# Kernel optimization log

Measured on AMD Instinct MI355X. Metric: run time of the kernel, lower is better.

The kernel has to match this reference:

```python
import jax, jax.numpy as jnp
import numpy as np

TEMP = 0.7
ALPHA_ADV = 1.0
BETA_BAND = 0.5
BAND_L = 0.05
BAND_H = 0.2
W_HEUR = 0.5
W_LEAR = 0.5


def setup_inputs() -> dict:
    key = jax.random.key(0)
    ks = jax.random.split(key, 6)
    B, Sn, C, H, W = 2, 5, 64, 192, 192
    hid = 64
    return {
        "S": jax.random.normal(ks[0], (B, C, H, W), jnp.float32),
        "T": jax.random.normal(ks[1], (B, Sn, C, H, W), jnp.float32),
        "adapt_w": jax.random.normal(ks[2], (Sn, C, C), jnp.float32) / np.sqrt(C).astype(np.float32),
        "adapt_b": jnp.zeros((Sn, C), jnp.float32),
        "r_w1": jax.random.normal(ks[3], (hid, Sn * C * 3), jnp.float32) * 0.05,
        "r_b1": jnp.zeros((hid,), jnp.float32),
        "r_w2": jax.random.normal(ks[4], (Sn, hid), jnp.float32) * 0.05,
        "r_b2": jnp.zeros((Sn,), jnp.float32),
        "ema_mu": jnp.zeros((1, Sn, C, 1, 1), jnp.float32),
        "ema_sigma": jnp.ones((1, Sn, C, 1, 1), jnp.float32),
        "ema_proxy": jnp.zeros((1, Sn, 1, 1, 1), jnp.float32),
    }


def reference(S, T, adapt_w, adapt_b, r_w1, r_b1, r_w2, r_b2, ema_mu, ema_sigma, ema_proxy):
    B, Sn, C, H, W = T.shape
    bias = adapt_b[None, :, :, None, None]
    # per-sweep 1x1 conv == per-sweep channel matmul
    T_adapt = jnp.einsum('sdc,bschw->bsdhw', adapt_w, T) + bias          # [B,S,C,H,W]
    S_rep = jnp.einsum('sdc,bchw->bsdhw', adapt_w, S) + bias             # [B,S,C,H,W]
    Tz = (T_adapt - ema_mu) / ema_sigma
    Sz = (S_rep - ema_mu) / ema_sigma
    delta = Tz - Sz
    proxy = jnp.mean(delta * delta, axis=2, keepdims=True)               # [B,S,1,H,W]
    cur = jnp.mean(proxy, axis=(0, 3, 4), keepdims=True)                 # [1,S,1,1,1]
    # heuristic score (gamma_ucb = 0 -> no UCB term)
    impr = jax.lax.stop_gradient(ema_proxy - cur)
    adv = impr - jnp.mean(impr, axis=1, keepdims=True)
    below = jnp.maximum(BAND_L - cur, 0.0)
    above = jnp.maximum(cur - BAND_H, 0.0)
    band = -(below * below + above * above)
    score = ALPHA_ADV * adv + BETA_BAND * band                           # [1,S,1,1,1]
    score_heur = jnp.broadcast_to(score, proxy.shape)[:, :, 0]           # [B,S,H,W]
    # learned router: concat along channel of each sweep then 1x1 MLP
    x = jnp.concatenate([Sz, Tz, delta], axis=2).reshape(B, Sn * 3 * C, H, W)
    h = jax.nn.relu(jnp.einsum('oi,bihw->bohw', r_w1, x) + r_b1[None, :, None, None])
    score_learn = jnp.einsum('oi,bihw->bohw', r_w2, h) + r_b2[None, :, None, None]
    logits = W_HEUR * score_heur + W_LEAR * score_learn                  # [B,S,H,W]
    weights = jax.nn.softmax(logits / TEMP, axis=1)                      # soft gating over sweeps
    return weights
```

## Files before the change

### kernel.cpp

```cpp
#include <hip/hip_runtime.h>
#include <math.h>

#define HWSZ 36864
#define NBLK4 1152

typedef short bf16x8 __attribute__((ext_vector_type(8)));
typedef float f32x16 __attribute__((ext_vector_type(16)));
typedef unsigned int u32x4 __attribute__((ext_vector_type(4)));

__device__ __forceinline__ unsigned short f2bf(float x) {
    unsigned u = __float_as_uint(x);
    return (unsigned short)((u + 0x7fffu + ((u >> 16) & 1u)) >> 16);
}

__device__ __forceinline__ void block_sync_lds() {
    __builtin_amdgcn_sched_barrier(0);
    asm volatile("s_waitcnt lgkmcnt(0)" ::: "memory");
    __builtin_amdgcn_s_barrier();
    __builtin_amdgcn_sched_barrier(0);
}

__global__ void pre_all(const float* __restrict__ rw1, const float* __restrict__ rb1,
                        const float* __restrict__ aw, const float* __restrict__ ab,
                        const float* __restrict__ mu, const float* __restrict__ sg,
                        unsigned short* __restrict__ AfragW,
                        unsigned short* __restrict__ AfragMS2, float* __restrict__ c1) {
    int i = blockIdx.x * 256 + threadIdx.x;
    if (i < 40960) {
        int s = i / 8192, rem = i % 8192;
        int r = rem / 2048, rem2 = rem % 2048;
        int t = rem2 / 512, q = rem2 % 512;
        int l = q >> 3, e = q & 7;
        int R = 32 * r + (l & 31);
        int k = 16 * t + 8 * (l >> 5) + e;
        float v;
        if (R < 64) {
            v = aw[s * 4096 + R * 64 + k] / sg[s * 64 + R];
        } else {
            int o = R - 64;
            const float* wp = rw1 + o * 960 + s * 192;
            const float* A  = aw + s * 4096 + k;
            const float* G  = sg + s * 64;
            float sum = 0.f;
            #pragma unroll 8
            for (int d = 0; d < 64; ++d)
                sum = fmaf(wp[64 + d] + wp[128 + d], A[d * 64] / G[d], sum);
            v = sum;
        }
        AfragW[i] = f2bf(v);
    } else if (i < 45056) {
        int j = i - 40960;
        int r = j / 2048, rem2 = j % 2048;
        int t = rem2 / 512, q = rem2 % 512;
        int l = q >> 3, e = q & 7;
        int o = 32 * r + (l & 31);
        int k = 16 * t + 8 * (l >> 5) + e;
        float sum = 0.f;
        for (int s = 0; s < 5; ++s) {
            const float* wp = rw1 + o * 960 + s * 192;
            const float* A  = aw + s * 4096 + k;
            const float* G  = sg + s * 64;
            #pragma unroll 8
            for (int d = 0; d < 64; ++d)
                sum = fmaf(wp[d] - wp[128 + d], A[d * 64] / G[d], sum);
        }
        AfragMS2[j] = f2bf(sum);
    } else if (i < 45120) {
        int o = i - 45056;
        float sum = rb1[o];
        for (int s = 0; s < 5; ++s) {
            const float* wp = rw1 + o * 960 + s * 192;
            #pragma unroll 8
            for (int d = 0; d < 64; ++d) {
                int sd = s * 64 + d;
                sum = fmaf(wp[d] + wp[64 + d], (ab[sd] - mu[sd]) / sg[sd], sum);
            }
        }
        c1[o] = sum;
    }
}

__global__ __launch_bounds__(256, 4) void fused_main(
        const float* __restrict__ S, const float* __restrict__ T,
        const unsigned short* __restrict__ AfragW, const unsigned short* __restrict__ AfragMS2,
        const float* __restrict__ c1, const float* __restrict__ rw2, const float* __restrict__ rb2,
        float* __restrict__ slearn, float* __restrict__ partial) {
    __shared__ __align__(16) unsigned short sTile[4096];
    __shared__ __align__(16) unsigned short tbuf[2][4096];
    __shared__ float hpart[2][5][64];
    __shared__ float wred[5][2];
    __shared__ float w2s[320];
    __shared__ float c1s[64];
    __shared__ float rb2s[8];

    const int tid = threadIdx.x, lane = tid & 63, w = tid >> 6;
    const int hi = lane >> 5, pxm = lane & 31;
    const int blk = blockIdx.x;
    const int b = blk / 576;
    const int pix0 = (blk % 576) * 64;

    const int o8 = tid >> 5, q = tid & 31;
    const int skt = o8 >> 1, shh = o8 & 1;
    const float* Sp = S + ((size_t)(b * 64 + 8 * o8)) * HWSZ + pix0 + 2 * q;
    const float* Tp = T + ((size_t)(b * 5 * 64 + 8 * o8)) * HWSZ + pix0 + 2 * q;

    float2 RS[8], RA[8], RB[8];
    #pragma unroll
    for (int j = 0; j < 8; ++j) RS[j] = *(const float2*)(Sp + (size_t)j * HWSZ);
    #pragma unroll
    for (int j = 0; j < 8; ++j) RA[j] = *(const float2*)(Tp + (size_t)j * HWSZ);
    #pragma unroll
    for (int j = 0; j < 8; ++j) RB[j] = *(const float2*)(Tp + (size_t)(64 + j) * HWSZ);

    for (int i = tid; i < 320; i += 256) w2s[i] = rw2[i];
    if (tid < 64) c1s[tid] = c1[tid];
    if (tid < 5)  rb2s[tid] = rb2[tid];

    auto packWrite = [&](unsigned short* dst, const float2* Rv) {
        #pragma unroll
        for (int h2 = 0; h2 < 2; ++h2) {
            int px = 2 * q + h2;
            int ct = px >> 5, slot = (px & 31) ^ ct;
            u32x4 v;
            #pragma unroll
            for (int jj = 0; jj < 4; ++jj) {
                float a = h2 ? Rv[2 * jj].y : Rv[2 * jj].x;
                float c = h2 ? Rv[2 * jj + 1].y : Rv[2 * jj + 1].x;
                v[jj] = (unsigned)f2bf(a) | ((unsigned)f2bf(c) << 16);
            }
            *(u32x4*)&dst[(((ct * 4 + skt) * 64) + shh * 32 + slot) * 8] = v;
        }
    };
    auto loadT = [&](float2* Rv, int s) {
        const float* p = Tp + (size_t)(s * 64) * HWSZ;
        #pragma unroll
        for (int j = 0; j < 8; ++j) Rv[j] = *(const float2*)(p + (size_t)j * HWSZ);
    };

    const bf16x8* afw = (const bf16x8*)AfragW + lane;
    bf16x8 fr0[4], fr1[4];
    #pragma unroll
    for (int kt = 0; kt < 4; ++kt) fr0[kt] = afw[((0 * 4 + w) * 4 + kt) * 64];

    packWrite(sTile, RS);
    block_sync_lds();

    auto ldsB = [&](const unsigned short* buf, int ct, int kt) -> bf16x8 {
        return *(const bf16x8*)&buf[(((ct * 4 + kt) * 64) + hi * 32 + (pxm ^ ct)) * 8];
    };

    f32x16 acc0, acc1;
    #pragma unroll
    for (int i = 0; i < 16; ++i) { acc0[i] = 0.f; acc1[i] = 0.f; }

    if (w >= 2) {
        const bf16x8* am = (const bf16x8*)AfragMS2 + lane;
        bf16x8 ms2f[4];
        #pragma unroll
        for (int kt = 0; kt < 4; ++kt) ms2f[kt] = am[((w - 2) * 4 + kt) * 64];
        #pragma unroll
        for (int kt = 0; kt < 4; ++kt) {
            acc0 = __builtin_amdgcn_mfma_f32_32x32x16_bf16(ms2f[kt], ldsB(sTile, 0, kt), acc0, 0, 0, 0);
            acc1 = __builtin_amdgcn_mfma_f32_32x32x16_bf16(ms2f[kt], ldsB(sTile, 1, kt), acc1, 0, 0, 0);
        }
    }

    packWrite(tbuf[0], RA);
    loadT(RA, 2);
    block_sync_lds();

    #pragma unroll
    for (int s = 0; s < 5; ++s) {
        const unsigned short* cur = tbuf[s & 1];
        unsigned short* nxt = tbuf[(s + 1) & 1];
        bf16x8* fcur = (s & 1) ? fr1 : fr0;
        bf16x8* fnxt = (s & 1) ? fr0 : fr1;
        if (s < 4) {
            #pragma unroll
            for (int kt = 0; kt < 4; ++kt) fnxt[kt] = afw[(((s + 1) * 4 + w) * 4 + kt) * 64];
        }
        if (w < 2) {
            #pragma unroll
            for (int i = 0; i < 16; ++i) { acc0[i] = 0.f; acc1[i] = 0.f; }
            #pragma unroll
            for (int kt = 0; kt < 4; ++kt) {
                acc0 = __builtin_amdgcn_mfma_f32_32x32x16_bf16(fcur[kt], ldsB(sTile, 0, kt), acc0, 0, 0, 0);
                acc1 = __builtin_amdgcn_mfma_f32_32x32x16_bf16(fcur[kt], ldsB(sTile, 1, kt), acc1, 0, 0, 0);
            }
            #pragma unroll
            for (int i = 0; i < 16; ++i) { acc0[i] = -acc0[i]; acc1[i] = -acc1[i]; }
            #pragma unroll
            for (int kt = 0; kt < 4; ++kt) {
                acc0 = __builtin_amdgcn_mfma_f32_32x32x16_bf16(fcur[kt], ldsB(cur, 0, kt), acc0, 0, 0, 0);
                acc1 = __builtin_amdgcn_mfma_f32_32x32x16_bf16(fcur[kt], ldsB(cur, 1, kt), acc1, 0, 0, 0);
            }
            float sq = 0.f;
            #pragma unroll
            for (int i = 0; i < 16; ++i) { sq = fmaf(acc0[i], acc0[i], sq); sq = fmaf(acc1[i], acc1[i], sq); }
            #pragma unroll
            for (int m = 1; m < 64; m <<= 1) sq += __shfl_xor(sq, m, 64);
            if (lane == 0) wred[s][w] = sq;
        } else {
            #pragma unroll
            for (int kt = 0; kt < 4; ++kt) {
                acc0 = __builtin_amdgcn_mfma_f32_32x32x16_bf16(fcur[kt], ldsB(cur, 0, kt), acc0, 0, 0, 0);
                acc1 = __builtin_amdgcn_mfma_f32_32x32x16_bf16(fcur[kt], ldsB(cur, 1, kt), acc1, 0, 0, 0);
            }
        }
        if (s < 4) {
            packWrite(nxt, (s & 1) ? RA : RB);
            if (s < 2) loadT((s & 1) ? RA : RB, s + 3);
        }
        block_sync_lds();
    }

    if (w >= 2) {
        #pragma unroll
        for (int i = 0; i < 16; ++i) {
            int row = (i & 3) + 8 * (i >> 2) + 4 * hi + 32 * (w - 2);
            acc0[i] = fmaxf(acc0[i] + c1s[row], 0.f);
            acc1[i] = fmaxf(acc1[i] + c1s[row], 0.f);
        }
        #pragma unroll
        for (int sp = 0; sp < 5; ++sp) {
            float d0 = 0.f, d1 = 0.f;
            #pragma unroll
            for (int i = 0; i < 16; ++i) {
                int row = (i & 3) + 8 * (i >> 2) + 4 * hi + 32 * (w - 2);
                d0 = fmaf(w2s[sp * 64 + row], acc0[i], d0);
                d1 = fmaf(w2s[sp * 64 + row], acc1[i], d1);
            }
            d0 += __shfl_xor(d0, 32, 64);
            d1 += __shfl_xor(d1, 32, 64);
            if (hi == 0) { hpart[w - 2][sp][pxm] = d0; hpart[w - 2][sp][32 + pxm] = d1; }
        }
    }
    block_sync_lds();
    if (tid < 5) partial[blk * 5 + tid] = wred[tid][0] + wred[tid][1];
    for (int i = tid; i < 320; i += 256) {
        int sp = i >> 6, px = i & 63;
        slearn[((size_t)(b * 5 + sp)) * HWSZ + pix0 + px] =
            hpart[0][sp][px] + hpart[1][sp][px] + rb2s[sp];
    }
}

__global__ void score_kernel(const float* __restrict__ partial,
                             const float* __restrict__ ema_proxy,
                             float* __restrict__ scoreBuf) {
    __shared__ float red[256];
    __shared__ float cur[5];
    int tid = threadIdx.x;
    for (int s = 0; s < 5; ++s) {
        float sum = 0.f;
        for (int i = tid; i < NBLK4; i += 256) sum += partial[i * 5 + s];
        red[tid] = sum;
        __syncthreads();
        for (int off = 128; off > 0; off >>= 1) {
            if (tid < off) red[tid] += red[tid + off];
            __syncthreads();
        }
        if (tid == 0) cur[s] = red[0] * (1.0f / (64.0f * 2.0f * HWSZ));
        __syncthreads();
    }
    if (tid == 0) {
        float impr[5]; float m = 0.f;
        for (int s = 0; s < 5; ++s) { impr[s] = ema_proxy[s] - cur[s]; m += impr[s]; }
        m *= 0.2f;
        for (int s = 0; s < 5; ++s) {
            float adv = impr[s] - m;
            float c = cur[s];
            float below = fmaxf(0.05f - c, 0.f);
            float above = fmaxf(c - 0.2f, 0.f);
            float band = -(below * below + above * above);
            scoreBuf[s] = 1.0f * adv + 0.5f * band;
        }
    }
}

__global__ void softmax_kernel(const float* __restrict__ slearn,
                               const float* __restrict__ scoreBuf,
                               float* __restrict__ out) {
    int i = blockIdx.x * 256 + threadIdx.x;
    if (i >= 2 * HWSZ) return;
    int b = i / HWSZ, p = i % HWSZ;
    float l[5];
    float mx = -1e30f;
    #pragma unroll
    for (int s = 0; s < 5; ++s) {
        float v = (0.5f * scoreBuf[s] + 0.5f * slearn[((size_t)(b * 5 + s)) * HWSZ + p]) / 0.7f;
        l[s] = v;
        mx = fmaxf(mx, v);
    }
    float sum = 0.f;
    #pragma unroll
    for (int s = 0; s < 5; ++s) { l[s] = expf(l[s] - mx); sum += l[s]; }
    float inv = 1.0f / sum;
    #pragma unroll
    for (int s = 0; s < 5; ++s) out[((size_t)(b * 5 + s)) * HWSZ + p] = l[s] * inv;
}

extern "C" void kernel_launch(void* const* d_in, const int* in_sizes, int n_in,
                              void* d_out, int out_size, void* d_ws, size_t ws_size,
                              hipStream_t stream) {
    const float* S   = (const float*)d_in[0];
    const float* T   = (const float*)d_in[1];
    const float* aw  = (const float*)d_in[2];
    const float* ab  = (const float*)d_in[3];
    const float* rw1 = (const float*)d_in[4];
    const float* rb1 = (const float*)d_in[5];
    const float* rw2 = (const float*)d_in[6];
    const float* rb2 = (const float*)d_in[7];
    const float* mu  = (const float*)d_in[8];
    const float* sg  = (const float*)d_in[9];
    const float* ep  = (const float*)d_in[10];

    float* ws = (float*)d_ws;
    float* c1f      = ws;
    float* scoreBuf = ws + 64;
    float* partial  = ws + 72;
    unsigned short* AfragW   = (unsigned short*)(ws + 5832);
    unsigned short* AfragMS2 = (unsigned short*)(ws + 26312);
    float* slearn   = ws + 28360;
    float* out = (float*)d_out;

    pre_all<<<177, 256, 0, stream>>>(rw1, rb1, aw, ab, mu, sg, AfragW, AfragMS2, c1f);
    fused_main<<<NBLK4, 256, 0, stream>>>(S, T, AfragW, AfragMS2, c1f, rw2, rb2, slearn, partial);
    score_kernel<<<1, 256, 0, stream>>>(partial, ep, scoreBuf);
    softmax_kernel<<<288, 256, 0, stream>>>(slearn, scoreBuf, out);
}
```

Before: 58.04 us.

## Double pixel tile per block to 128 with float4 loads and 4 MFMA accumulators

Each block of the fused kernel now covers 128 pixels instead of 64. That halves the grid to 576 blocks and gives each block four 32-pixel MFMA column tiles, so every loaded weight fragment feeds four MFMAs instead of two. Global loads widen from float2 to float4, and the T prefetch drops from two register buffers to a single rotating buffer. LDS roughly doubles, hpart is aliased onto tbuf, and launch bounds fall to 3 blocks per SM, which reduces occupancy and the number of blocks available to spread across the device.

```diff
diff --git a/kernel.cpp b/kernel.cpp
--- a/kernel.cpp
+++ b/kernel.cpp
@@ -2,7 +2,8 @@
 #include <math.h>
 
 #define HWSZ 36864
-#define NBLK4 1152
+#define NPX  128
+#define NBLK5 576
 
 typedef short bf16x8 __attribute__((ext_vector_type(8)));
 typedef float f32x16 __attribute__((ext_vector_type(16)));
@@ -80,14 +81,13 @@
     }
 }
 
-__global__ __launch_bounds__(256, 4) void fused_main(
+__global__ __launch_bounds__(256, 3) void fused_main(
         const float* __restrict__ S, const float* __restrict__ T,
         const unsigned short* __restrict__ AfragW, const unsigned short* __restrict__ AfragMS2,
         const float* __restrict__ c1, const float* __restrict__ rw2, const float* __restrict__ rb2,
         float* __restrict__ slearn, float* __restrict__ partial) {
-    __shared__ __align__(16) unsigned short sTile[4096];
-    __shared__ __align__(16) unsigned short tbuf[2][4096];
-    __shared__ float hpart[2][5][64];
+    __shared__ __align__(16) unsigned short sTile[8192];
+    __shared__ __align__(16) unsigned short tbuf[2][8192];
     __shared__ float wred[5][2];
     __shared__ float w2s[320];
     __shared__ float c1s[64];
@@ -96,45 +96,43 @@
     const int tid = threadIdx.x, lane = tid & 63, w = tid >> 6;
     const int hi = lane >> 5, pxm = lane & 31;
     const int blk = blockIdx.x;
-    const int b = blk / 576;
-    const int pix0 = (blk % 576) * 64;
+    const int b = blk / 288;
+    const int pix0 = (blk % 288) * NPX;
 
     const int o8 = tid >> 5, q = tid & 31;
     const int skt = o8 >> 1, shh = o8 & 1;
-    const float* Sp = S + ((size_t)(b * 64 + 8 * o8)) * HWSZ + pix0 + 2 * q;
-    const float* Tp = T + ((size_t)(b * 5 * 64 + 8 * o8)) * HWSZ + pix0 + 2 * q;
-
-    float2 RS[8], RA[8], RB[8];
-    #pragma unroll
-    for (int j = 0; j < 8; ++j) RS[j] = *(const float2*)(Sp + (size_t)j * HWSZ);
-    #pragma unroll
-    for (int j = 0; j < 8; ++j) RA[j] = *(const float2*)(Tp + (size_t)j * HWSZ);
-    #pragma unroll
-    for (int j = 0; j < 8; ++j) RB[j] = *(const float2*)(Tp + (size_t)(64 + j) * HWSZ);
+    const float* Sp = S + ((size_t)(b * 64 + 8 * o8)) * HWSZ + pix0 + 4 * q;
+    const float* Tp = T + ((size_t)(b * 5 * 64 + 8 * o8)) * HWSZ + pix0 + 4 * q;
+
+    float4 RS[8], RA[8];
+    #pragma unroll
+    for (int j = 0; j < 8; ++j) RS[j] = *(const float4*)(Sp + (size_t)j * HWSZ);
+    #pragma unroll
+    for (int j = 0; j < 8; ++j) RA[j] = *(const float4*)(Tp + (size_t)j * HWSZ);
 
     for (int i = tid; i < 320; i += 256) w2s[i] = rw2[i];
     if (tid < 64) c1s[tid] = c1[tid];
     if (tid < 5)  rb2s[tid] = rb2[tid];
 
-    auto packWrite = [&](unsigned short* dst, const float2* Rv) {
-        #pragma unroll
-        for (int h2 = 0; h2 < 2; ++h2) {
-            int px = 2 * q + h2;
+    auto packWrite = [&](unsigned short* dst, const float4* Rv) {
+        #pragma unroll
+        for (int pi = 0; pi < 4; ++pi) {
+            int px = 4 * q + pi;
             int ct = px >> 5, slot = (px & 31) ^ ct;
             u32x4 v;
             #pragma unroll
             for (int jj = 0; jj < 4; ++jj) {
-                float a = h2 ? Rv[2 * jj].y : Rv[2 * jj].x;
-                float c = h2 ? Rv[2 * jj + 1].y : Rv[2 * jj + 1].x;
+                float a = ((const float*)&Rv[2 * jj])[pi];
+                float c = ((const float*)&Rv[2 * jj + 1])[pi];
                 v[jj] = (unsigned)f2bf(a) | ((unsigned)f2bf(c) << 16);
             }
             *(u32x4*)&dst[(((ct * 4 + skt) * 64) + shh * 32 + slot) * 8] = v;
         }
     };
-    auto loadT = [&](float2* Rv, int s) {
+    auto loadT = [&](float4* Rv, int s) {
         const float* p = Tp + (size_t)(s * 64) * HWSZ;
         #pragma unroll
-        for (int j = 0; j < 8; ++j) Rv[j] = *(const float2*)(p + (size_t)j * HWSZ);
+        for (int j = 0; j < 8; ++j) Rv[j] = *(const float4*)(p + (size_t)j * HWSZ);
     };
 
     const bf16x8* afw = (const bf16x8*)AfragW + lane;
@@ -149,9 +147,11 @@
         return *(const bf16x8*)&buf[(((ct * 4 + kt) * 64) + hi * 32 + (pxm ^ ct)) * 8];
     };
 
-    f32x16 acc0, acc1;
-    #pragma unroll
-    for (int i = 0; i < 16; ++i) { acc0[i] = 0.f; acc1[i] = 0.f; }
+    f32x16 acc[4];
+    #pragma unroll
+    for (int n = 0; n < 4; ++n)
+        #pragma unroll
+        for (int i = 0; i < 16; ++i) acc[n][i] = 0.f;
 
     if (w >= 2) {
         const bf16x8* am = (const bf16x8*)AfragMS2 + lane;
@@ -159,14 +159,14 @@
         #pragma unroll
         for (int kt = 0; kt < 4; ++kt) ms2f[kt] = am[((w - 2) * 4 + kt) * 64];
         #pragma unroll
-        for (int kt = 0; kt < 4; ++kt) {
-            acc0 = __builtin_amdgcn_mfma_f32_32x32x16_bf16(ms2f[kt], ldsB(sTile, 0, kt), acc0, 0, 0, 0);
-            acc1 = __builtin_amdgcn_mfma_f32_32x32x16_bf16(ms2f[kt], ldsB(sTile, 1, kt), acc1, 0, 0, 0);
-        }
+        for (int kt = 0; kt < 4; ++kt)
+            #pragma unroll
+            for (int n = 0; n < 4; ++n)
+                acc[n] = __builtin_amdgcn_mfma_f32_32x32x16_bf16(ms2f[kt], ldsB(sTile, n, kt), acc[n], 0, 0, 0);
     }
 
     packWrite(tbuf[0], RA);
-    loadT(RA, 2);
+    loadT(RA, 1);
     block_sync_lds();
 
     #pragma unroll
@@ -181,66 +181,74 @@
         }
         if (w < 2) {
             #pragma unroll
-            for (int i = 0; i < 16; ++i) { acc0[i] = 0.f; acc1[i] = 0.f; }
-            #pragma unroll
-            for (int kt = 0; kt < 4; ++kt) {
-                acc0 = __builtin_amdgcn_mfma_f32_32x32x16_bf16(fcur[kt], ldsB(sTile, 0, kt), acc0, 0, 0, 0);
-                acc1 = __builtin_amdgcn_mfma_f32_32x32x16_bf16(fcur[kt], ldsB(sTile, 1, kt), acc1, 0, 0, 0);
-            }
-            #pragma unroll
-            for (int i = 0; i < 16; ++i) { acc0[i] = -acc0[i]; acc1[i] = -acc1[i]; }
-            #pragma unroll
-            for (int kt = 0; kt < 4; ++kt) {
-                acc0 = __builtin_amdgcn_mfma_f32_32x32x16_bf16(fcur[kt], ldsB(cur, 0, kt), acc0, 0, 0, 0);
-                acc1 = __builtin_amdgcn_mfma_f32_32x32x16_bf16(fcur[kt], ldsB(cur, 1, kt), acc1, 0, 0, 0);
-            }
+            for (int n = 0; n < 4; ++n)
+                #pragma unroll
+                for (int i = 0; i < 16; ++i) acc[n][i] = 0.f;
+            #pragma unroll
+            for (int kt = 0; kt < 4; ++kt)
+                #pragma unroll
+                for (int n = 0; n < 4; ++n)
+                    acc[n] = __builtin_amdgcn_mfma_f32_32x32x16_bf16(fcur[kt], ldsB(sTile, n, kt), acc[n], 0, 0, 0);
+            #pragma unroll
+            for (int n = 0; n < 4; ++n)
+                #pragma unroll
+                for (int i = 0; i < 16; ++i) acc[n][i] = -acc[n][i];
+            #pragma unroll
+            for (int kt = 0; kt < 4; ++kt)
+                #pragma unroll
+                for (int n = 0; n < 4; ++n)
+                    acc[n] = __builtin_amdgcn_mfma_f32_32x32x16_bf16(fcur[kt], ldsB(cur, n, kt), acc[n], 0, 0, 0);
             float sq = 0.f;
             #pragma unroll
-            for (int i = 0; i < 16; ++i) { sq = fmaf(acc0[i], acc0[i], sq); sq = fmaf(acc1[i], acc1[i], sq); }
+            for (int n = 0; n < 4; ++n)
+                #pragma unroll
+                for (int i = 0; i < 16; ++i) sq = fmaf(acc[n][i], acc[n][i], sq);
             #pragma unroll
             for (int m = 1; m < 64; m <<= 1) sq += __shfl_xor(sq, m, 64);
             if (lane == 0) wred[s][w] = sq;
         } else {
             #pragma unroll
-            for (int kt = 0; kt < 4; ++kt) {
-                acc0 = __builtin_amdgcn_mfma_f32_32x32x16_bf16(fcur[kt], ldsB(cur, 0, kt), acc0, 0, 0, 0);
-                acc1 = __builtin_amdgcn_mfma_f32_32x32x16_bf16(fcur[kt], ldsB(cur, 1, kt), acc1, 0, 0, 0);
-            }
+            for (int kt = 0; kt < 4; ++kt)
+                #pragma unroll
+                for (int n = 0; n < 4; ++n)
+                    acc[n] = __builtin_amdgcn_mfma_f32_32x32x16_bf16(fcur[kt], ldsB(cur, n, kt), acc[n], 0, 0, 0);
         }
         if (s < 4) {
-            packWrite(nxt, (s & 1) ? RA : RB);
-            if (s < 2) loadT((s & 1) ? RA : RB, s + 3);
+            packWrite(nxt, RA);
+            if (s < 3) loadT(RA, s + 2);
         }
         block_sync_lds();
     }
 
+    float* hpart = (float*)tbuf;
     if (w >= 2) {
         #pragma unroll
-        for (int i = 0; i < 16; ++i) {
-            int row = (i & 3) + 8 * (i >> 2) + 4 * hi + 32 * (w - 2);
-            acc0[i] = fmaxf(acc0[i] + c1s[row], 0.f);
-            acc1[i] = fmaxf(acc1[i] + c1s[row], 0.f);
-        }
-        #pragma unroll
-        for (int sp = 0; sp < 5; ++sp) {
-            float d0 = 0.f, d1 = 0.f;
+        for (int n = 0; n < 4; ++n)
             #pragma unroll
             for (int i = 0; i < 16; ++i) {
                 int row = (i & 3) + 8 * (i >> 2) + 4 * hi + 32 * (w - 2);
-                d0 = fmaf(w2s[sp * 64 + row], acc0[i], d0);
-                d1 = fmaf(w2s[sp * 64 + row], acc1[i], d1);
+                acc[n][i] = fmaxf(acc[n][i] + c1s[row], 0.f);
             }
-            d0 += __shfl_xor(d0, 32, 64);
-            d1 += __shfl_xor(d1, 32, 64);
-            if (hi == 0) { hpart[w - 2][sp][pxm] = d0; hpart[w - 2][sp][32 + pxm] = d1; }
-        }
+        #pragma unroll
+        for (int sp = 0; sp < 5; ++sp)
+            #pragma unroll
+            for (int n = 0; n < 4; ++n) {
+                float d = 0.f;
+                #pragma unroll
+                for (int i = 0; i < 16; ++i) {
+                    int row = (i & 3) + 8 * (i >> 2) + 4 * hi + 32 * (w - 2);
+                    d = fmaf(w2s[sp * 64 + row], acc[n][i], d);
+                }
+                d += __shfl_xor(d, 32, 64);
+                if (hi == 0) hpart[(w - 2) * 640 + sp * 128 + n * 32 + pxm] = d;
+            }
     }
     block_sync_lds();
     if (tid < 5) partial[blk * 5 + tid] = wred[tid][0] + wred[tid][1];
-    for (int i = tid; i < 320; i += 256) {
-        int sp = i >> 6, px = i & 63;
+    for (int i = tid; i < 640; i += 256) {
+        int sp = i >> 7, px = i & 127;
         slearn[((size_t)(b * 5 + sp)) * HWSZ + pix0 + px] =
-            hpart[0][sp][px] + hpart[1][sp][px] + rb2s[sp];
+            hpart[sp * 128 + px] + hpart[640 + sp * 128 + px] + rb2s[sp];
     }
 }
 
@@ -252,7 +260,7 @@
     int tid = threadIdx.x;
     for (int s = 0; s < 5; ++s) {
         float sum = 0.f;
-        for (int i = tid; i < NBLK4; i += 256) sum += partial[i * 5 + s];
+        for (int i = tid; i < NBLK5; i += 256) sum += partial[i * 5 + s];
         red[tid] = sum;
         __syncthreads();
         for (int off = 128; off > 0; off >>= 1) {
@@ -324,7 +332,7 @@
     float* out = (float*)d_out;
 
     pre_all<<<177, 256, 0, stream>>>(rw1, rb1, aw, ab, mu, sg, AfragW, AfragMS2, c1f);
-    fused_main<<<NBLK4, 256, 0, stream>>>(S, T, AfragW, AfragMS2, c1f, rw2, rb2, slearn, partial);
+    fused_main<<<NBLK5, 256, 0, stream>>>(S, T, AfragW, AfragMS2, c1f, rw2, rb2, slearn, partial);
     score_kernel<<<1, 256, 0, stream>>>(partial, ep, scoreBuf);
     softmax_kernel<<<288, 256, 0, stream>>>(slearn, scoreBuf, out);
 }
```

New measurement: 60.01 us. 1.03x slower.

## Halve per-block pixel tile and give each wave both delta and MLP work

Applied to the files above, without the earlier changes.

The main fused kernel now uses 128-thread blocks covering 32 pixels each and launches twice as many blocks. Previously two waves computed the delta/proxy path and two the hidden-layer path. Now each wave does both for its half of the output rows, reusing the S tile held in registers and sharing each T fragment load between the two MFMA chains. The aim is more blocks in flight, balanced wave work and lower register/LDS pressure. The cost is reloading A fragments every sweep without prefetch, twice the per-block overhead, and twice as many partial sums for the score reduction.

```diff
diff --git a/kernel.cpp b/kernel.cpp
--- a/kernel.cpp
+++ b/kernel.cpp
@@ -2,7 +2,7 @@
 #include <math.h>
 
 #define HWSZ 36864
-#define NBLK4 1152
+#define NWID 2304
 
 typedef short bf16x8 __attribute__((ext_vector_type(8)));
 typedef float f32x16 __attribute__((ext_vector_type(16)));
@@ -80,55 +80,53 @@
     }
 }
 
-__global__ __launch_bounds__(256, 4) void fused_main(
+__global__ __launch_bounds__(128, 4) void fused_main(
         const float* __restrict__ S, const float* __restrict__ T,
         const unsigned short* __restrict__ AfragW, const unsigned short* __restrict__ AfragMS2,
         const float* __restrict__ c1, const float* __restrict__ rw2, const float* __restrict__ rb2,
         float* __restrict__ slearn, float* __restrict__ partial) {
-    __shared__ __align__(16) unsigned short sTile[4096];
-    __shared__ __align__(16) unsigned short tbuf[2][4096];
-    __shared__ float hpart[2][5][64];
-    __shared__ float wred[5][2];
+    __shared__ __align__(16) unsigned short sTile[2048];
+    __shared__ __align__(16) unsigned short tbuf[2][2048];
     __shared__ float w2s[320];
     __shared__ float c1s[64];
     __shared__ float rb2s[8];
+    __shared__ float wred[5][2];
+    __shared__ float hpart[2][5][32];
 
     const int tid = threadIdx.x, lane = tid & 63, w = tid >> 6;
     const int hi = lane >> 5, pxm = lane & 31;
     const int blk = blockIdx.x;
-    const int b = blk / 576;
-    const int pix0 = (blk % 576) * 64;
-
-    const int o8 = tid >> 5, q = tid & 31;
-    const int skt = o8 >> 1, shh = o8 & 1;
-    const float* Sp = S + ((size_t)(b * 64 + 8 * o8)) * HWSZ + pix0 + 2 * q;
-    const float* Tp = T + ((size_t)(b * 5 * 64 + 8 * o8)) * HWSZ + pix0 + 2 * q;
-
-    float2 RS[8], RA[8], RB[8];
+    const int b = blk / 1152;
+    const int pix0 = (blk % 1152) * 32;
+
+    const int o8 = tid >> 4, pq = tid & 15;
+    const float* Sp = S + ((size_t)(b * 64 + 8 * o8)) * HWSZ + pix0 + 2 * pq;
+    const float* Tp = T + ((size_t)(b * 5 * 64 + 8 * o8)) * HWSZ + pix0 + 2 * pq;
+
+    float2 RS[8], R[8];
     #pragma unroll
     for (int j = 0; j < 8; ++j) RS[j] = *(const float2*)(Sp + (size_t)j * HWSZ);
     #pragma unroll
-    for (int j = 0; j < 8; ++j) RA[j] = *(const float2*)(Tp + (size_t)j * HWSZ);
-    #pragma unroll
-    for (int j = 0; j < 8; ++j) RB[j] = *(const float2*)(Tp + (size_t)(64 + j) * HWSZ);
-
-    for (int i = tid; i < 320; i += 256) w2s[i] = rw2[i];
+    for (int j = 0; j < 8; ++j) R[j] = *(const float2*)(Tp + (size_t)j * HWSZ);
+
+    for (int i = tid; i < 320; i += 128) w2s[i] = rw2[i];
     if (tid < 64) c1s[tid] = c1[tid];
     if (tid < 5)  rb2s[tid] = rb2[tid];
 
+    auto slot = [](int px) { return px ^ (px >> 3); };
+
     auto packWrite = [&](unsigned short* dst, const float2* Rv) {
         #pragma unroll
-        for (int h2 = 0; h2 < 2; ++h2) {
-            int px = 2 * q + h2;
-            int ct = px >> 5, slot = (px & 31) ^ ct;
+        for (int pi = 0; pi < 2; ++pi) {
+            int px = 2 * pq + pi;
             u32x4 v;
             #pragma unroll
             for (int jj = 0; jj < 4; ++jj) {
-                float a = h2 ? Rv[2 * jj].y : Rv[2 * jj].x;
-                float c = h2 ? Rv[2 * jj + 1].y : Rv[2 * jj + 1].x;
+                float a = pi ? Rv[2 * jj].y : Rv[2 * jj].x;
+                float c = pi ? Rv[2 * jj + 1].y : Rv[2 * jj + 1].x;
                 v[jj] = (unsigned)f2bf(a) | ((unsigned)f2bf(c) << 16);
             }
-            *(u32x4*)&dst[(((ct * 4 + skt) * 64) + shh * 32 + slot) * 8] = v;
+            *(u32x4*)&dst[(o8 * 32 + slot(px)) * 8] = v;
         }
     };
     auto loadT = [&](float2* Rv, int s) {
@@ -136,109 +134,96 @@
         #pragma unroll
         for (int j = 0; j < 8; ++j) Rv[j] = *(const float2*)(p + (size_t)j * HWSZ);
     };
-
-    const bf16x8* afw = (const bf16x8*)AfragW + lane;
-    bf16x8 fr0[4], fr1[4];
-    #pragma unroll
-    for (int kt = 0; kt < 4; ++kt) fr0[kt] = afw[((0 * 4 + w) * 4 + kt) * 64];
+    auto ldsB = [&](const unsigned short* buf, int kt) -> bf16x8 {
+        return *(const bf16x8*)&buf[((kt * 2 + hi) * 32 + slot(pxm)) * 8];
+    };
+
+    const bf16x8* am = (const bf16x8*)AfragMS2 + lane;
+    bf16x8 msf[4];
+    #pragma unroll
+    for (int kt = 0; kt < 4; ++kt) msf[kt] = am[(w * 4 + kt) * 64];
 
     packWrite(sTile, RS);
     block_sync_lds();
 
-    auto ldsB = [&](const unsigned short* buf, int ct, int kt) -> bf16x8 {
-        return *(const bf16x8*)&buf[(((ct * 4 + kt) * 64) + hi * 32 + (pxm ^ ct)) * 8];
-    };
-
-    f32x16 acc0, acc1;
-    #pragma unroll
-    for (int i = 0; i < 16; ++i) { acc0[i] = 0.f; acc1[i] = 0.f; }
-
-    if (w >= 2) {
-        const bf16x8* am = (const bf16x8*)AfragMS2 + lane;
-        bf16x8 ms2f[4];
-        #pragma unroll
-        for (int kt = 0; kt < 4; ++kt) ms2f[kt] = am[((w - 2) * 4 + kt) * 64];
-        #pragma unroll
-        for (int kt = 0; kt < 4; ++kt) {
-            acc0 = __builtin_amdgcn_mfma_f32_32x32x16_bf16(ms2f[kt], ldsB(sTile, 0, kt), acc0, 0, 0, 0);
-            acc1 = __builtin_amdgcn_mfma_f32_32x32x16_bf16(ms2f[kt], ldsB(sTile, 1, kt), acc1, 0, 0, 0);
-        }
-    }
-
-    packWrite(tbuf[0], RA);
-    loadT(RA, 2);
+    bf16x8 bS[4];
+    #pragma unroll
+    for (int kt = 0; kt < 4; ++kt) bS[kt] = ldsB(sTile, kt);
+
+    f32x16 hacc;
+    #pragma unroll
+    for (int i = 0; i < 16; ++i) hacc[i] = 0.f;
+    #pragma unroll
+    for (int kt = 0; kt < 4; ++kt)
+        hacc = __builtin_amdgcn_mfma_f32_32x32x16_bf16(msf[kt], bS[kt], hacc, 0, 0, 0);
+
+    packWrite(tbuf[0], R);
+    loadT(R, 1);
     block_sync_lds();
+
+    const bf16x8* afw = (const bf16x8*)AfragW + lane;
 
     #pragma unroll
     for (int s = 0; s < 5; ++s) {
         const unsigned short* cur = tbuf[s & 1];
         unsigned short* nxt = tbuf[(s + 1) & 1];
-        bf16x8* fcur = (s & 1) ? fr1 : fr0;
-        bf16x8* fnxt = (s & 1) ? fr0 : fr1;
+
+        bf16x8 fD[4], fM[4];
+        #pragma unroll
+        for (int kt = 0; kt < 4; ++kt) fD[kt] = afw[((s * 4 + w) * 4 + kt) * 64];
+        #pragma unroll
+        for (int kt = 0; kt < 4; ++kt) fM[kt] = afw[((s * 4 + 2 + w) * 4 + kt) * 64];
+
         if (s < 4) {
-            #pragma unroll
-            for (int kt = 0; kt < 4; ++kt) fnxt[kt] = afw[(((s + 1) * 4 + w) * 4 + kt) * 64];
-        }
-        if (w < 2) {
-            #pragma unroll
-            for (int i = 0; i < 16; ++i) { acc0[i] = 0.f; acc1[i] = 0.f; }
-            #pragma unroll
-            for (int kt = 0; kt < 4; ++kt) {
-                acc0 = __builtin_amdgcn_mfma_f32_32x32x16_bf16(fcur[kt], ldsB(sTile, 0, kt), acc0, 0, 0, 0);
-                acc1 = __builtin_amdgcn_mfma_f32_32x32x16_bf16(fcur[kt], ldsB(sTile, 1, kt), acc1, 0, 0, 0);
-            }
-            #pragma unroll
-            for (int i = 0; i < 16; ++i) { acc0[i] = -acc0[i]; acc1[i] = -acc1[i]; }
-            #pragma unroll
-            for (int kt = 0; kt < 4; ++kt) {
-                acc0 = __builtin_amdgcn_mfma_f32_32x32x16_bf16(fcur[kt], ldsB(cur, 0, kt), acc0, 0, 0, 0);
-                acc1 = __builtin_amdgcn_mfma_f32_32x32x16_bf16(fcur[kt], ldsB(cur, 1, kt), acc1, 0, 0, 0);
-            }
-            float sq = 0.f;
-            #pragma unroll
-            for (int i = 0; i < 16; ++i) { sq = fmaf(acc0[i], acc0[i], sq); sq = fmaf(acc1[i], acc1[i], sq); }
-            #pragma unroll
-            for (int m = 1; m < 64; m <<= 1) sq += __shfl_xor(sq, m, 64);
-            if (lane == 0) wred[s][w] = sq;
-        } else {
-            #pragma unroll
-            for (int kt = 0; kt < 4; ++kt) {
-                acc0 = __builtin_amdgcn_mfma_f32_32x32x16_bf16(fcur[kt], ldsB(cur, 0, kt), acc0, 0, 0, 0);
-                acc1 = __builtin_amdgcn_mfma_f32_32x32x16_bf16(fcur[kt], ldsB(cur, 1, kt), acc1, 0, 0, 0);
-            }
-        }
-        if (s < 4) {
-            packWrite(nxt, (s & 1) ? RA : RB);
-            if (s < 2) loadT((s & 1) ? RA : RB, s + 3);
-        }
+            packWrite(nxt, R);
+            if (s < 3) loadT(R, s + 2);
+        }
+
+        f32x16 dacc;
+        #pragma unroll
+        for (int i = 0; i < 16; ++i) dacc[i] = 0.f;
+        #pragma unroll
+        for (int kt = 0; kt < 4; ++kt)
+            dacc = __builtin_amdgcn_mfma_f32_32x32x16_bf16(fD[kt], bS[kt], dacc, 0, 0, 0);
+        #pragma unroll
+        for (int i = 0; i < 16; ++i) dacc[i] = -dacc[i];
+        #pragma unroll
+        for (int kt = 0; kt < 4; ++kt) {
+            bf16x8 bT = ldsB(cur, kt);
+            dacc = __builtin_amdgcn_mfma_f32_32x32x16_bf16(fD[kt], bT, dacc, 0, 0, 0);
+            hacc = __builtin_amdgcn_mfma_f32_32x32x16_bf16(fM[kt], bT, hacc, 0, 0, 0);
+        }
+
+        float sq = 0.f;
+        #pragma unroll
+        for (int i = 0; i < 16; ++i) sq = fmaf(dacc[i], dacc[i], sq);
+        #pragma unroll
+        for (int m = 1; m < 64; m <<= 1) sq += __shfl_xor(sq, m, 64);
+        if (lane == 0) wred[s][w] = sq;
+
         block_sync_lds();
     }
 
-    if (w >= 2) {
+    #pragma unroll
+    for (int i = 0; i < 16; ++i) {
+        int row = (i & 3) + 8 * (i >> 2) + 4 * hi + 32 * w;
+        hacc[i] = fmaxf(hacc[i] + c1s[row], 0.f);
+    }
+    #pragma unroll
+    for (int sp = 0; sp < 5; ++sp) {
+        float d = 0.f;
         #pragma unroll
         for (int i = 0; i < 16; ++i) {
-            int row = (i & 3) + 8 * (i >> 2) + 4 * hi + 32 * (w - 2);
-            acc0[i] = fmaxf(acc0[i] + c1s[row], 0.f);
-            acc1[i] = fmaxf(acc1[i] + c1s[row], 0.f);
-        }
-        #pragma unroll
-        for (int sp = 0; sp < 5; ++sp) {
-            float d0 = 0.f, d1 = 0.f;
-            #pragma unroll
-            for (int i = 0; i < 16; ++i) {
-                int row = (i & 3) + 8 * (i >> 2) + 4 * hi + 32 * (w - 2);
-                d0 = fmaf(w2s[sp * 64 + row], acc0[i], d0);
-                d1 = fmaf(w2s[sp * 64 + row], acc1[i], d1);
-            }
-            d0 += __shfl_xor(d0, 32, 64);
-            d1 += __shfl_xor(d1, 32, 64);
-            if (hi == 0) { hpart[w - 2][sp][pxm] = d0; hpart[w - 2][sp][32 + pxm] = d1; }
-        }
+            int row = (i & 3) + 8 * (i >> 2) + 4 * hi + 32 * w;
+            d = fmaf(w2s[sp * 64 + row], hacc[i], d);
+        }
+        d += __shfl_xor(d, 32, 64);
+        if (hi == 0) hpart[w][sp][pxm] = d;
     }
     block_sync_lds();
     if (tid < 5) partial[blk * 5 + tid] = wred[tid][0] + wred[tid][1];
-    for (int i = tid; i < 320; i += 256) {
-        int sp = i >> 6, px = i & 63;
+    for (int i = tid; i < 160; i += 128) {
+        int sp = i >> 5, px = i & 31;
         slearn[((size_t)(b * 5 + sp)) * HWSZ + pix0 + px] =
             hpart[0][sp][px] + hpart[1][sp][px] + rb2s[sp];
     }
@@ -252,7 +237,7 @@
     int tid = threadIdx.x;
     for (int s = 0; s < 5; ++s) {
         float sum = 0.f;
-        for (int i = tid; i < NBLK4; i += 256) sum += partial[i * 5 + s];
+        for (int i = tid; i < NWID; i += 256) sum += partial[i * 5 + s];
         red[tid] = sum;
         __syncthreads();
         for (int off = 128; off > 0; off >>= 1) {
@@ -318,13 +303,13 @@
     float* c1f      = ws;
     float* scoreBuf = ws + 64;
     float* partial  = ws + 72;
-    unsigned short* AfragW   = (unsigned short*)(ws + 5832);
-    unsigned short* AfragMS2 = (unsigned short*)(ws + 26312);
-    float* slearn   = ws + 28360;
+    unsigned short* AfragW   = (unsigned short*)(ws + 11592);
+    unsigned short* AfragMS2 = (unsigned short*)(ws + 32072);
+    float* slearn   = ws + 34120;
     float* out = (float*)d_out;
 
     pre_all<<<177, 256, 0, stream>>>(rw1, rb1, aw, ab, mu, sg, AfragW, AfragMS2, c1f);
-    fused_main<<<NBLK4, 256, 0, stream>>>(S, T, AfragW, AfragMS2, c1f, rw2, rb2, slearn, partial);
+    fused_main<<<NWID, 128, 0, stream>>>(S, T, AfragW, AfragMS2, c1f, rw2, rb2, slearn, partial);
     score_kernel<<<1, 256, 0, stream>>>(partial, ep, scoreBuf);
     softmax_kernel<<<288, 256, 0, stream>>>(slearn, scoreBuf, out);
 }
```

Result: slower. 66.04 us (+13.8%).
